# Kernel tuning notes

Measured on AMD Instinct MI355X. Metric: run time of the kernel, lower is better.

## Reference

```python
import jax, jax.numpy as jnp
import numpy as np

SCORE = 89; PERF = 300; R = SCORE + PERF   # roll_dims = score_1hot + perf_1hot
H = 1024; Z = 256; B = 64; T = 256
DUR, DY, IOI = 0, 100, 200                 # perf segment boundaries (durratio/dy/ioi)
BN_EPS = 1e-5

PARAM_SHAPES = [
    ("w_ih_f", (3*H, R)), ("w_hh_f", (3*H, H)), ("b_ih_f", (3*H,)), ("b_hh_f", (3*H,)),
    ("w_ih_b", (3*H, R)), ("w_hh_b", (3*H, H)), ("b_ih_b", (3*H,)), ("b_hh_b", (3*H,)),
    ("w_mu", (Z, 2*H)), ("b_mu", (Z,)), ("w_var", (Z, 2*H)), ("b_var", (Z,)),
    ("w_init", (H, Z)), ("b_init", (H,)),
    ("w_ih0", (3*H, Z + R)), ("w_hh0", (3*H, H)), ("b_ih0", (3*H,)), ("b_hh0", (3*H,)),
    ("w_ih1", (3*H, H)), ("w_hh1", (3*H, H)), ("b_ih1", (3*H,)), ("b_hh1", (3*H,)),
    ("w_ih2", (3*H, H)), ("w_hh2", (3*H, H)), ("b_ih2", (3*H,)), ("b_hh2", (3*H,)),
    ("w_out", (PERF, H)), ("b_out", (PERF,)),
]


def gru_cell(x, h, w_ih, w_hh, b_ih, b_hh):
    # torch GRU/GRUCell gate order: r, z, n
    gi = x @ w_ih.T + b_ih
    gh = h @ w_hh.T + b_hh
    i_r, i_z, i_n = jnp.split(gi, 3, axis=-1)
    h_r, h_z, h_n = jnp.split(gh, 3, axis=-1)
    r = jax.nn.sigmoid(i_r + h_r)
    zg = jax.nn.sigmoid(i_z + h_z)
    n = jnp.tanh(i_n + r * h_n)
    return (1.0 - zg) * n + zg * h


def setup_inputs() -> dict:
    key = jax.random.key(0)
    ks = jax.random.split(key, len(PARAM_SHAPES) + 1)
    inp = {"x": jax.random.normal(ks[0], (T, B, R), dtype=jnp.float32),
           "x_lengths": T}
    for i, (nm, shp) in enumerate(PARAM_SHAPES):
        inp[nm] = jax.random.normal(ks[i + 1], shp, dtype=jnp.float32) * 0.05
    return inp


def _forward(x, w_ih_f, w_hh_f, b_ih_f, b_hh_f, w_ih_b, w_hh_b, b_ih_b, b_hh_b,
             w_mu, b_mu, w_var, b_var, w_init, b_init,
             w_ih0, w_hh0, b_ih0, b_hh0, w_ih1, w_hh1, b_ih1, b_hh1,
             w_ih2, w_hh2, b_ih2, b_hh2, w_out, b_out):
    # ---- encode: bidirectional GRU, all lengths == T (pack == plain GRU) ----
    h0 = jnp.zeros((B, H), x.dtype)
    def run(xs, w_ih, w_hh, b_ih, b_hh):
        step = lambda h, xt: ((gru_cell(xt, h, w_ih, w_hh, b_ih, b_hh),) * 2)
        hT, _ = jax.lax.scan(step, h0, xs)
        return hT
    h_f = run(x, w_ih_f, w_hh_f, b_ih_f, b_hh_f)
    h_b = run(x[::-1], w_ih_b, w_hh_b, b_ih_b, b_hh_b)
    hidden = jnp.concatenate([h_f, h_b], axis=-1)          # [B, 2H]
    hidden = hidden / jnp.sqrt(1.0 + BN_EPS)               # BatchNorm2d(1) eval, fresh running stats
    mean = hidden @ w_mu.T + b_mu
    stddev = jnp.exp((hidden @ w_var.T + b_var) * 0.5)     # computed as in torch (unused in eval)
    z = mean                                               # eval-mode reparameterize -> mean
    score = x[:, :, :SCORE]                                # [T, B, SCORE]
    out0 = jnp.zeros((B, PERF), x.dtype).at[:, -1].set(1.0)
    sc0 = jnp.zeros((B, SCORE), x.dtype).at[:, -1].set(1.0)
    hinit = jnp.tanh(z @ w_init.T + b_init)                # hx[0] init
    def step(carry, xj):
        out, sc, hx0, hx1, hx2 = carry
        j, score_j = xj
        inp = jnp.concatenate([out, sc, z], axis=1)        # [B, PERF+SCORE+Z]
        hx0 = gru_cell(inp, hx0, w_ih0, w_hh0, b_ih0, b_hh0)
        hx1 = gru_cell(hx0, jnp.where(j == 0, hx0, hx1), w_ih1, w_hh1, b_ih1, b_hh1)
        hx2 = gru_cell(hx1, jnp.where(j == 0, hx1, hx2), w_ih2, w_hh2, b_ih2, b_hh2)
        logits = hx2 @ w_out.T + b_out                     # [B, PERF]
        o = jnp.concatenate([jax.nn.log_softmax(logits[:, DUR:DY], axis=1),
                             jax.nn.log_softmax(logits[:, DY:IOI], axis=1),
                             jax.nn.log_softmax(logits[:, IOI:], axis=1)], axis=1)
        out_next = jax.nn.one_hot(jnp.argmax(o, axis=1), PERF, dtype=o.dtype)  # eval sampling
        return (out_next, score_j, hx0, hx1, hx2), o
    _, outs = jax.lax.scan(step, (out0, sc0, hinit, hinit, hinit),
                           (jnp.arange(T), score))
    return outs.transpose(1, 0, 2)                         # [B, T, PERF]


def reference(x, x_lengths, w_ih_f, w_hh_f, b_ih_f, b_hh_f, w_ih_b, w_hh_b, b_ih_b, b_hh_b,
              w_mu, b_mu, w_var, b_var, w_init, b_init,
              w_ih0, w_hh0, b_ih0, b_hh0, w_ih1, w_hh1, b_ih1, b_hh1,
              w_ih2, w_hh2, b_ih2, b_hh2, w_out, b_out):
    outs = _forward(x, w_ih_f, w_hh_f, b_ih_f, b_hh_f, w_ih_b, w_hh_b, b_ih_b, b_hh_b,
                    w_mu, b_mu, w_var, b_var, w_init, b_init,
                    w_ih0, w_hh0, b_ih0, b_hh0, w_ih1, w_hh1, b_ih1, b_hh1,
                    w_ih2, w_hh2, b_ih2, b_hh2, w_out, b_out)
    zeros = jnp.zeros((B, Z), x.dtype)  # dis_mean / dis_stddev stay zero in eval branch
    return outs, zeros, zeros
```

## Files before the change

kernel.cpp:

```cpp
#include <hip/hip_runtime.h>
#include <math.h>

namespace {

typedef unsigned long long u64;

constexpr int cH  = 1024;
constexpr int cZ  = 256;
constexpr int cB  = 64;
constexpr int cT  = 256;
constexpr int cR  = 389;
constexpr int cSC = 89;
constexpr int cPF = 300;
constexpr int WSTR = 400;
constexpr float INV_S = 0.9999950000374997f;

__device__ __forceinline__ void fma4(float4& a, const float4 x, const float4 w){
  a.x = fmaf(x.x, w.x, a.x);
  a.y = fmaf(x.y, w.y, a.y);
  a.z = fmaf(x.z, w.z, a.z);
  a.w = fmaf(x.w, w.w, a.w);
}
__device__ __forceinline__ float fold4(const float4 a){ return (a.x + a.y) + (a.z + a.w); }
__device__ __forceinline__ float4 z4(){ return make_float4(0.f, 0.f, 0.f, 0.f); }
__device__ __forceinline__ float sigm(float x){ return 1.f / (1.f + expf(-x)); }

__device__ __forceinline__ void cfence(){ asm volatile("" ::: "memory"); }
__device__ __forceinline__ u64 ld_u64(const u64* p){
  return __hip_atomic_load(p, __ATOMIC_RELAXED, __HIP_MEMORY_SCOPE_AGENT);
}
__device__ __forceinline__ float ld_scal(const float* p){
  return __hip_atomic_load(p, __ATOMIC_RELAXED, __HIP_MEMORY_SCOPE_AGENT);
}
__device__ __forceinline__ void st_scal(float* p, float v){
  __hip_atomic_store(p, v, __ATOMIC_RELAXED, __HIP_MEMORY_SCOPE_AGENT);
}

__device__ __forceinline__ void gbarN(unsigned* base, int sub, unsigned subCnt,
                                      int nsub, unsigned rootCnt){
  __syncthreads();
  if (threadIdx.x == 0){
    cfence();
    unsigned* root = base + nsub * 16;
    unsigned* gen  = base + nsub * 16 + 16;
    const unsigned g = __hip_atomic_load(gen, __ATOMIC_RELAXED, __HIP_MEMORY_SCOPE_AGENT);
    const unsigned a = __hip_atomic_fetch_add(base + sub * 16, 1u,
                         __ATOMIC_RELEASE, __HIP_MEMORY_SCOPE_AGENT);
    bool flip = false;
    if (a == subCnt - 1u){
      const unsigned r = __hip_atomic_fetch_add(root, 1u,
                           __ATOMIC_RELEASE, __HIP_MEMORY_SCOPE_AGENT);
      if (r == rootCnt - 1u){
        for (int t = 0; t < nsub; ++t)
          __hip_atomic_store(base + t * 16, 0u, __ATOMIC_RELAXED, __HIP_MEMORY_SCOPE_AGENT);
        __hip_atomic_store(root, 0u, __ATOMIC_RELAXED, __HIP_MEMORY_SCOPE_AGENT);
        __hip_atomic_store(gen, g + 1u, __ATOMIC_RELEASE, __HIP_MEMORY_SCOPE_AGENT);
        flip = true;
      }
    }
    if (!flip){
      while (__hip_atomic_load(gen, __ATOMIC_RELAXED, __HIP_MEMORY_SCOPE_AGENT) == g)
        __builtin_amdgcn_s_sleep(1);
    }
    cfence();
  }
  __syncthreads();
}

__global__ __launch_bounds__(256) void init_kernel(float* hf0, float* hb0, float* dout_tail,
                                                   unsigned* barE, unsigned* barD){
  const int idx = blockIdx.x * 256 + threadIdx.x;
  const int stride = gridDim.x * 256;
  for (int i = idx; i < cB * cH; i += stride){ hf0[i] = 0.f; hb0[i] = 0.f; }
  for (int i = idx; i < 2 * cB * cZ; i += stride) dout_tail[i] = 0.f;
  for (int i = idx; i < 2048; i += stride) barE[i] = 0u;
  for (int i = idx; i < 512;  i += stride) barD[i] = 0u;
}

__global__ __launch_bounds__(256) void pad_wih_kernel(const float* __restrict__ w,
                                                      float* __restrict__ wp){
  const int idx = blockIdx.x * 256 + threadIdx.x;
  const int stride = gridDim.x * 256;
  const int n = 3 * cH * WSTR;
  for (int i = idx; i < n; i += stride){
    const int r = i / WSTR, c = i - r * WSTR;
    wp[i] = (c < cR) ? w[(size_t)r * cR + c] : 0.f;
  }
}

__global__ __launch_bounds__(256) void pad_wsc_kernel(const float* __restrict__ w_ih0,
                                                      float* __restrict__ wsc){
  const int idx = blockIdx.x * 256 + threadIdx.x;
  const int stride = gridDim.x * 256;
  const int n = 3 * cH * 96;
  for (int i = idx; i < n; i += stride){
    const int r = i / 96, c = i - r * 96;
    wsc[i] = (c < cSC) ? w_ih0[(size_t)r * 645 + 300 + c] : 0.f;
  }
}

__global__ __launch_bounds__(512, 2) void enc_persist(
    const float* __restrict__ x,
    const float* __restrict__ wihPf, const float* __restrict__ whh_f,
    const float* __restrict__ bih_f, const float* __restrict__ bhh_f,
    const float* __restrict__ wihPb, const float* __restrict__ whh_b,
    const float* __restrict__ bih_b, const float* __restrict__ bhh_b,
    float* __restrict__ hfA, float* __restrict__ hfB,
    float* __restrict__ hbA, float* __restrict__ hbB,
    unsigned* __restrict__ barE)
{
  const int bid   = blockIdx.x;
  const int xcd   = bid & 7;
  const int slot  = bid >> 3;
  const int dir   = slot >> 4;
  const int sub16 = slot & 15;
  const int kblk  = xcd * 8 + (sub16 >> 1);
  const int bhalf = sub16 & 1;
  unsigned* bar   = barE + (dir * 2 + bhalf) * 512;

  const float* wih = dir ? wihPb : wihPf;
  const float* whh = dir ? whh_b : whh_f;
  const float* bih = dir ? bih_b : bih_f;
  const float* bhh = dir ? bhh_b : bhh_f;
  float* bufA = dir ? hbA : hfA;
  float* bufB = dir ? hbB : hfB;

  const int tid   = threadIdx.x;
  const int seg8  = tid >> 6;
  const int dseg  = seg8 & 3;
  const int khalf = seg8 >> 2;
  const int lane  = tid & 63;
  const int tx    = lane & 7;
  const int ty    = lane >> 3;
  const int k0    = kblk * 16;
  const int bbase = bhalf * 32;
  const int kloc  = khalf * 8 + ty;
  const int k     = k0 + kloc;

  __shared__ float part[4][4][16][33];
  __shared__ alignas(16) float sh[32 * 516];

  const float4* w0i = (const float4*)wih + (size_t)k * 100;
  const float4* w1i = (const float4*)wih + (size_t)(cH + k) * 100;
  const float4* w2i = (const float4*)wih + (size_t)(2*cH + k) * 100;
  const float4* w0h = (const float4*)whh + (size_t)k * 256;
  const float4* w1h = (const float4*)whh + (size_t)(cH + k) * 256;
  const float4* w2h = (const float4*)whh + (size_t)(2*cH + k) * 256;
  float4* sh4 = (float4*)sh;

  auto stageE = [&](const float* hin, int p){
    const u64* s8 = (const u64*)hin;
    u64* d8 = (u64*)sh;
    u64 tmp[16];
    #pragma unroll
    for (int i = 0; i < 16; ++i){
      const int e = i * 512 + tid;
      tmp[i] = ld_u64(s8 + (size_t)(bbase + (e >> 8)) * 512 + p * 256 + (e & 255));
    }
    #pragma unroll
    for (int i = 0; i < 16; ++i){
      const int e = i * 512 + tid;
      d8[(e >> 8) * 258 + (e & 255)] = tmp[i];
    }
  };

  for (int t = 0; t < cT; ++t){
    const float* hin = (t & 1) ? bufB : bufA;
    float*      hout = (t & 1) ? bufA : bufB;
    const int tt = dir ? (cT - 1 - t) : t;

    float4 R[4], Z[4], NI[4], NH[4];
    #pragma unroll
    for (int jj = 0; jj < 4; ++jj){ R[jj]=z4(); Z[jj]=z4(); NI[jj]=z4(); NH[jj]=z4(); }

    {
      const float* xb[4];
      #pragma unroll
      for (int jj = 0; jj < 4; ++jj)
        xb[jj] = x + ((size_t)tt * cB + bbase + tx + 8*jj) * cR;
      const int c0 = dseg * 25;
      const int cEnd = c0 + 25;
      const int cSafe = (cEnd < 97) ? cEnd : 97;
      for (int c = c0; c < cSafe; ++c){
        const float4 w0v = w0i[c], w1v = w1i[c], w2v = w2i[c];
        const int d = 4 * c;
        #pragma unroll
        for (int jj = 0; jj < 4; ++jj){
          const float* xr = xb[jj];
          const float4 a = make_float4(xr[d], xr[d+1], xr[d+2], xr[d+3]);
          fma4(R[jj], a, w0v); fma4(Z[jj], a, w1v); fma4(NI[jj], a, w2v);
        }
      }
      for (int c = cSafe; c < cEnd; ++c){
        const float4 w0v = w0i[c], w1v = w1i[c], w2v = w2i[c];
        const int d = 4 * c;
        #pragma unroll
        for (int jj = 0; jj < 4; ++jj){
          const float* xr = xb[jj];
          const float4 a = make_float4(
              (d   < cR) ? xr[d]   : 0.f, (d+1 < cR) ? xr[d+1] : 0.f,
              (d+2 < cR) ? xr[d+2] : 0.f, (d+3 < cR) ? xr[d+3] : 0.f);
          fma4(R[jj], a, w0v); fma4(Z[jj], a, w1v); fma4(NI[jj], a, w2v);
        }
      }
    }

    #pragma unroll 1
    for (int p = 0; p < 2; ++p){
      stageE(hin, p);
      __syncthreads();
      {
        const float4* wp0 = w0h + p * 128;
        const float4* wp1 = w1h + p * 128;
        const float4* wp2 = w2h + p * 128;
        #pragma unroll 4
        for (int c = 0; c < 32; ++c){
          const int cc = dseg * 32 + c;
          const float4 w0v = wp0[cc], w1v = wp1[cc], w2v = wp2[cc];
          #pragma unroll
          for (int jj = 0; jj < 4; ++jj){
            const float4 a = sh4[(tx + 8*jj)*129 + cc];
            fma4(R[jj], a, w0v); fma4(Z[jj], a, w1v); fma4(NH[jj], a, w2v);
          }
        }
      }
      __syncthreads();
    }

    #pragma unroll
    for (int jj = 0; jj < 4; ++jj){
      const int b = tx + 8*jj;
      part[dseg][0][kloc][b] = fold4(R[jj]);
      part[dseg][1][kloc][b] = fold4(Z[jj]);
      part[dseg][2][kloc][b] = fold4(NI[jj]);
      part[dseg][3][kloc][b] = fold4(NH[jj]);
    }
    __syncthreads();
    {
      const int row = tid >> 5, bb = tid & 31;
      float rs=0.f, zs=0.f, nis=0.f, nhs=0.f;
      #pragma unroll
      for (int s = 0; s < 4; ++s){
        rs += part[s][0][row][bb]; zs += part[s][1][row][bb];
        nis += part[s][2][row][bb]; nhs += part[s][3][row][bb];
      }
      const int kk = k0 + row, gb = bbase + bb;
      const float r  = sigm(rs + bih[kk] + bhh[kk]);
      const float zg = sigm(zs + bih[cH + kk] + bhh[cH + kk]);
      const float nn = tanhf(nis + bih[2*cH + kk] + r * (nhs + bhh[2*cH + kk]));
      const float hp = ld_scal(&hin[(size_t)gb * cH + kk]);
      st_scal(&hout[(size_t)gb * cH + kk], (1.f - zg) * nn + zg * hp);
    }
    gbarN(bar, kblk >> 3, 8u, 8, 8u);
  }
}

__global__ __launch_bounds__(512, 2) void dec_persist(
    const float* __restrict__ x,
    const float* __restrict__ hfA, const float* __restrict__ hbA,
    const float* __restrict__ w_mu, const float* __restrict__ b_mu,
    const float* __restrict__ w_init, const float* __restrict__ b_init,
    const float* __restrict__ w_ih0,
    const float* __restrict__ wsc,   const float* __restrict__ w_hh0,
    const float* __restrict__ b_ih0, const float* __restrict__ b_hh0,
    const float* __restrict__ w_ih1, const float* __restrict__ w_hh1,
    const float* __restrict__ b_ih1, const float* __restrict__ b_hh1,
    const float* __restrict__ w_ih2, const float* __restrict__ w_hh2,
    const float* __restrict__ b_ih2, const float* __restrict__ b_hh2,
    const float* __restrict__ w_out, const float* __restrict__ b_out,
    float* __restrict__ h0A, float* __restrict__ h0B,
    float* __restrict__ h1A, float* __restrict__ h1B,
    float* __restrict__ h2A, float* __restrict__ h2B,
    float* __restrict__ gi0z, float* __restrict__ zbuf,
    float* __restrict__ amg,  float* __restrict__ scg,
    float* __restrict__ dout,
    unsigned* __restrict__ barD)
{
  const int bid  = blockIdx.x;
  const int xcd  = bid & 7;
  const int slot = bid >> 3;
  const int kq   = xcd * 16 + (slot >> 1);
  const int bh   = slot & 1;
  const int kbase = kq * 8;
  const int bbase = bh * 32;
  const int tid = threadIdx.x;

  const int seg  = tid >> 6;
  const int lane = tid & 63;
  const int tx   = lane & 7;
  const int ty   = lane >> 3;
  const int k    = kbase + ty;

  __shared__ float part[8][4][8][33];
  __shared__ alignas(16) float stg[16 * 1028];
  __shared__ alignas(16) float scs[32 * 100];
  __shared__ float ams[32];
  __shared__ alignas(16) float hb2[cH];
  __shared__ float lg[cPF];
  __shared__ float gmax[3], glse[3], wbest[8];
  __shared__ int   wbidx[8];

  float4* stg4 = (float4*)stg;

  #define GBD gbarN(barD, bid >> 4, 16u, 16, 16u)

  auto stageH = [&](const float* src, int gb0){
    const u64* s8 = (const u64*)src;
    u64* d8 = (u64*)stg;
    u64 tmp[16];
    #pragma unroll
    for (int i = 0; i < 16; ++i){
      const int e = i * 512 + tid;
      tmp[i] = ld_u64(s8 + (size_t)(gb0 + (e >> 9)) * 512 + (e & 511));
    }
    #pragma unroll
    for (int i = 0; i < 16; ++i){
      const int e = i * 512 + tid;
      d8[(e >> 9) * 514 + (e & 511)] = tmp[i];
    }
  };

  auto accH = [&](const float4* w0, const float4* w1, const float4* w2,
                  float4& A0, float4& A1, float4& B0, float4& B1,
                  float4& C0, float4& C1){
    #pragma unroll 4
    for (int c = 0; c < 32; ++c){
      const int cc = seg * 32 + c;
      const float4 w0v = w0[cc], w1v = w1[cc], w2v = w2[cc];
      const float4 aA = stg4[tx * 257 + cc];
      const float4 aB = stg4[(tx + 8) * 257 + cc];
      fma4(A0, aA, w0v); fma4(B0, aA, w1v); fma4(C0, aA, w2v);
      fma4(A1, aB, w0v); fma4(B1, aB, w1v); fma4(C1, aB, w2v);
    }
  };

  auto reduce_store = [&](const float* bi, const float* bhv,
                          const float* hprev, float* hout){
    __syncthreads();
    if (tid < 256){
      const int row = tid >> 5, b = tid & 31;
      float rs=0.f, zs=0.f, nis=0.f, nhs=0.f;
      #pragma unroll
      for (int s = 0; s < 8; ++s){
        rs += part[s][0][row][b]; zs += part[s][1][row][b];
        nis += part[s][2][row][b]; nhs += part[s][3][row][b];
      }
      const int kk = kbase + row, gb = bbase + b;
      const float r  = sigm(rs + bi[kk] + bhv[kk]);
      const float zg = sigm(zs + bi[cH + kk] + bhv[cH + kk]);
      const float nn = tanhf(nis + bi[2*cH + kk] + r * (nhs + bhv[2*cH + kk]));
      const float hp = ld_scal(&hprev[(size_t)gb * cH + kk]);
      st_scal(&hout[(size_t)gb * cH + kk], (1.f - zg) * nn + zg * hp);
    }
  };

  if (bid < cB){
    const int b = bid;
    float4* hl4 = (float4*)stg;
    hl4[tid] = (tid < 256) ? ((const float4*)hfA)[(size_t)b * 256 + tid]
                           : ((const float4*)hbA)[(size_t)b * 256 + (tid - 256)];
    __syncthreads();
    if (tid < 256){
      const float4* wr = (const float4*)w_mu + (size_t)tid * 512;
      float4 s = z4();
      #pragma unroll 4
      for (int c = 0; c < 512; ++c) fma4(s, hl4[c], wr[c]);
      st_scal(&zbuf[(size_t)b * cZ + tid], b_mu[tid] + fold4(s) * INV_S);
    }
    if (tid == 0) st_scal(&amg[b], 299.f);
    if (tid < 96) st_scal(&scg[(size_t)b * 96 + tid], (tid == 88) ? 1.f : 0.f);
  }
  GBD;
  {
    float* zl = stg;
    {
      u64 tmp[8];
      const u64* zb8 = (const u64*)zbuf;
      u64* zl8 = (u64*)stg;
      #pragma unroll
      for (int q = 0; q < 8; ++q){
        const int e = q * 512 + tid;
        tmp[q] = ld_u64(zb8 + (size_t)(bbase + (e >> 7)) * 128 + (e & 127));
      }
      #pragma unroll
      for (int q = 0; q < 8; ++q){
        const int e = q * 512 + tid;
        zl8[(e >> 7) * 130 + (e & 127)] = tmp[q];
      }
    }
    __syncthreads();
    for (int e = tid; e < 768; e += 512){
      const int g = e >> 8, kr = (e >> 5) & 7, b = e & 31;
      const float* zr = zl + b * 260;
      const float* wrow = w_ih0 + (size_t)(g * cH + kbase + kr) * 645 + 389;
      float s = 0.f;
      #pragma unroll 4
      for (int d = 0; d < cZ; ++d) s = fmaf(zr[d], wrow[d], s);
      st_scal(&gi0z[(size_t)(g * cH + kbase + kr) * 64 + bbase + b], s);
    }
    if (tid < 256){
      const int kr = tid >> 5, b = tid & 31;
      const float4* zr4 = (const float4*)(zl + b * 260);
      const float4* wr4 = (const float4*)w_init + (size_t)(kbase + kr) * 64;
      float4 s = z4();
      #pragma unroll 4
      for (int d = 0; d < 64; ++d) fma4(s, zr4[d], wr4[d]);
      st_scal(&h0A[(size_t)(bbase + b) * cH + kbase + kr],
              tanhf(b_init[kbase + kr] + fold4(s)));
    }
  }
  GBD;

  for (int j = 0; j < cT; ++j){
    const int par = j & 1;
    const float* h0p = par ? h0B : h0A;  float* h0n = par ? h0A : h0B;
    const float* h1p = par ? h1B : h1A;  float* h1n = par ? h1A : h1B;
    const float* h2p = par ? h2B : h2A;  float* h2n = par ? h2A : h2B;

    {
      {
        u64 tmp[3];
        const u64* sg8 = (const u64*)scg;
        u64* sc8 = (u64*)scs;
        #pragma unroll
        for (int i = 0; i < 3; ++i){
          const int e = i * 512 + tid;
          const int row = e / 48, col = e - row * 48;
          tmp[i] = ld_u64(sg8 + (size_t)(bbase + row) * 48 + col);
        }
        #pragma unroll
        for (int i = 0; i < 3; ++i){
          const int e = i * 512 + tid;
          const int row = e / 48, col = e - row * 48;
          sc8[row * 50 + col] = tmp[i];
        }
        if (tid < 32) ams[tid] = ld_scal(&amg[bbase + tid]);
      }
      __syncthreads();

      float4 R[4], Z[4], NI[4], NH[4];
      float sR[4], sZ[4], sNI[4];
      #pragma unroll
      for (int jj = 0; jj < 4; ++jj){
        R[jj]=z4(); Z[jj]=z4(); NI[jj]=z4(); NH[jj]=z4();
        sR[jj]=0.f; sZ[jj]=0.f; sNI[jj]=0.f;
      }
      {
        const float4* ws0 = (const float4*)wsc + (size_t)k * 24;
        const float4* ws1 = (const float4*)wsc + (size_t)(cH + k) * 24;
        const float4* ws2 = (const float4*)wsc + (size_t)(2*cH + k) * 24;
        const float4* sc4 = (const float4*)scs;
        #pragma unroll
        for (int c = 0; c < 3; ++c){
          const int cc = seg * 3 + c;
          const float4 w0v = ws0[cc], w1v = ws1[cc], w2v = ws2[cc];
          #pragma unroll
          for (int jj = 0; jj < 4; ++jj){
            const float4 a = sc4[(tx + 8*jj) * 25 + cc];
            fma4(R[jj], a, w0v); fma4(Z[jj], a, w1v); fma4(NI[jj], a, w2v);
          }
        }
      }
      if (seg == 0){
        #pragma unroll
        for (int jj = 0; jj < 4; ++jj){
          const int b = tx + 8*jj, gb = bbase + b;
          const int am = (int)ams[b];
          sR[jj]  = w_ih0[(size_t)k * 645 + am]
                  + ld_scal(&gi0z[(size_t)k * 64 + gb]);
          sZ[jj]  = w_ih0[(size_t)(cH + k) * 645 + am]
                  + ld_scal(&gi0z[(size_t)(cH + k) * 64 + gb]);
          sNI[jj] = w_ih0[(size_t)(2*cH + k) * 645 + am]
                  + ld_scal(&gi0z[(size_t)(2*cH + k) * 64 + gb]);
        }
      }
      const float4* wh0 = (const float4*)w_hh0 + (size_t)k * 256;
      const float4* wh1 = (const float4*)w_hh0 + (size_t)(cH + k) * 256;
      const float4* wh2 = (const float4*)w_hh0 + (size_t)(2*cH + k) * 256;
      __syncthreads();
      stageH(h0p, bbase);      __syncthreads();
      accH(wh0, wh1, wh2, R[0], R[1], Z[0], Z[1], NH[0], NH[1]);
      __syncthreads();
      stageH(h0p, bbase + 16); __syncthreads();
      accH(wh0, wh1, wh2, R[2], R[3], Z[2], Z[3], NH[2], NH[3]);
      #pragma unroll
      for (int jj = 0; jj < 4; ++jj){
        const int b = tx + 8*jj;
        part[seg][0][ty][b] = fold4(R[jj]) + sR[jj];
        part[seg][1][ty][b] = fold4(Z[jj]) + sZ[jj];
        part[seg][2][ty][b] = fold4(NI[jj]) + sNI[jj];
        part[seg][3][ty][b] = fold4(NH[jj]);
      }
      reduce_store(b_ih0, b_hh0, h0p, h0n);
    }
    GBD;

    #pragma unroll 1
    for (int L = 0; L < 2; ++L){
      const float* inG = (L == 0) ? h0n : h1n;
      const float* pvG = (L == 0) ? (j == 0 ? h0n : h1p) : (j == 0 ? h1n : h2p);
      const float* wih = (L == 0) ? w_ih1 : w_ih2;
      const float* whh = (L == 0) ? w_hh1 : w_hh2;
      const float* bi  = (L == 0) ? b_ih1 : b_ih2;
      const float* bhv = (L == 0) ? b_hh1 : b_hh2;
      float* outG      = (L == 0) ? h1n : h2n;

      float4 R[4], Z[4], NI[4], NH[4];
      #pragma unroll
      for (int jj = 0; jj < 4; ++jj){ R[jj]=z4(); Z[jj]=z4(); NI[jj]=z4(); NH[jj]=z4(); }
      const float4* wi0 = (const float4*)wih + (size_t)k * 256;
      const float4* wi1 = (const float4*)wih + (size_t)(cH + k) * 256;
      const float4* wi2 = (const float4*)wih + (size_t)(2*cH + k) * 256;
      const float4* wh0 = (const float4*)whh + (size_t)k * 256;
      const float4* wh1 = (const float4*)whh + (size_t)(cH + k) * 256;
      const float4* wh2 = (const float4*)whh + (size_t)(2*cH + k) * 256;

      stageH(inG, bbase);      __syncthreads();
      accH(wi0, wi1, wi2, R[0], R[1], Z[0], Z[1], NI[0], NI[1]);
      __syncthreads();
      stageH(inG, bbase + 16); __syncthreads();
      accH(wi0, wi1, wi2, R[2], R[3], Z[2], Z[3], NI[2], NI[3]);
      __syncthreads();
      stageH(pvG, bbase);      __syncthreads();
      accH(wh0, wh1, wh2, R[0], R[1], Z[0], Z[1], NH[0], NH[1]);
      __syncthreads();
      stageH(pvG, bbase + 16); __syncthreads();
      accH(wh0, wh1, wh2, R[2], R[3], Z[2], Z[3], NH[2], NH[3]);
      #pragma unroll
      for (int jj = 0; jj < 4; ++jj){
        const int b = tx + 8*jj;
        part[seg][0][ty][b] = fold4(R[jj]);
        part[seg][1][ty][b] = fold4(Z[jj]);
        part[seg][2][ty][b] = fold4(NI[jj]);
        part[seg][3][ty][b] = fold4(NH[jj]);
      }
      reduce_store(bi, bhv, pvG, outG);
      GBD;
    }

    if (bid < cB){
      const int b = bid;
      ((u64*)hb2)[tid] = ld_u64((const u64*)h2n + (size_t)b * 512 + tid);
      __syncthreads();
      for (int p = tid; p < cPF; p += 512){
        const float4* wr = (const float4*)w_out + (size_t)p * 256;
        const float4* hv = (const float4*)hb2;
        float4 s = z4();
        #pragma unroll 4
        for (int c = 0; c < 256; ++c) fma4(s, hv[c], wr[c]);
        lg[p] = b_out[p] + fold4(s);
      }
      __syncthreads();
      const int w = tid >> 6, l = tid & 63;
      if (w < 3){
        float m = -INFINITY;
        for (int p = w*100 + l; p < w*100 + 100; p += 64) m = fmaxf(m, lg[p]);
        #pragma unroll
        for (int off = 32; off > 0; off >>= 1) m = fmaxf(m, __shfl_xor(m, off));
        float s = 0.f;
        for (int p = w*100 + l; p < w*100 + 100; p += 64) s += expf(lg[p] - m);
        #pragma unroll
        for (int off = 32; off > 0; off >>= 1) s += __shfl_xor(s, off);
        if (l == 0){ gmax[w] = m; glse[w] = logf(s); }
      }
      __syncthreads();
      float best = -INFINITY; int bidx = 0x7fffffff;
      for (int p = tid; p < cPF; p += 512){
        const int g3 = (p >= 200) ? 2 : ((p >= 100) ? 1 : 0);
        const float o = lg[p] - gmax[g3] - glse[g3];
        dout[((size_t)b * cT + j) * cPF + p] = o;
        if (o > best || (o == best && p < bidx)){ best = o; bidx = p; }
      }
      #pragma unroll
      for (int off = 32; off > 0; off >>= 1){
        const float ob = __shfl_xor(best, off);
        const int   oi = __shfl_xor(bidx, off);
        if (ob > best || (ob == best && oi < bidx)){ best = ob; bidx = oi; }
      }
      if (l == 0){ wbest[w] = best; wbidx[w] = bidx; }
      __syncthreads();
      if (tid == 0){
        float bb = wbest[0]; int bi = wbidx[0];
        #pragma unroll
        for (int q = 1; q < 8; ++q)
          if (wbest[q] > bb || (wbest[q] == bb && wbidx[q] < bi)){ bb = wbest[q]; bi = wbidx[q]; }
        st_scal(&amg[b], (float)bi);
      }
      if (tid < 96)
        st_scal(&scg[(size_t)b * 96 + tid],
                (tid < cSC) ? x[((size_t)j * cB + b) * cR + tid] : 0.f);
    }
    GBD;
  }
  #undef GBD
}

}

extern "C" void kernel_launch(void* const* d_in, const int* in_sizes, int n_in,
                              void* d_out, int out_size, void* d_ws, size_t ws_size,
                              hipStream_t stream)
{
  const float* x     = (const float*)d_in[0];
  const float* wih_f = (const float*)d_in[2];
  const float* whh_f = (const float*)d_in[3];
  const float* bih_f = (const float*)d_in[4];
  const float* bhh_f = (const float*)d_in[5];
  const float* wih_b = (const float*)d_in[6];
  const float* whh_b = (const float*)d_in[7];
  const float* bih_b = (const float*)d_in[8];
  const float* bhh_b = (const float*)d_in[9];
  const float* w_mu  = (const float*)d_in[10];
  const float* b_mu  = (const float*)d_in[11];
  const float* w_init= (const float*)d_in[14];
  const float* b_init= (const float*)d_in[15];
  const float* w_ih0 = (const float*)d_in[16];
  const float* w_hh0 = (const float*)d_in[17];
  const float* b_ih0 = (const float*)d_in[18];
  const float* b_hh0 = (const float*)d_in[19];
  const float* w_ih1 = (const float*)d_in[20];
  const float* w_hh1 = (const float*)d_in[21];
  const float* b_ih1 = (const float*)d_in[22];
  const float* b_hh1 = (const float*)d_in[23];
  const float* w_ih2 = (const float*)d_in[24];
  const float* w_hh2 = (const float*)d_in[25];
  const float* b_ih2 = (const float*)d_in[26];
  const float* b_hh2 = (const float*)d_in[27];
  const float* w_out = (const float*)d_in[28];
  const float* b_out = (const float*)d_in[29];
  float* dout = (float*)d_out;

  float* ws = (float*)d_ws;
  float* wihfP = ws; ws += (size_t)3 * cH * WSTR;
  float* wihbP = ws; ws += (size_t)3 * cH * WSTR;
  float* wsc   = ws; ws += (size_t)3 * cH * 96;
  float* gi0z  = ws; ws += (size_t)3 * cH * 64;
  float* hfA = ws; ws += cB * cH;  float* hfB = ws; ws += cB * cH;
  float* hbA = ws; ws += cB * cH;  float* hbB = ws; ws += cB * cH;
  float* h0A = ws; ws += cB * cH;  float* h0B = ws; ws += cB * cH;
  float* h1A = ws; ws += cB * cH;  float* h1B = ws; ws += cB * cH;
  float* h2A = ws; ws += cB * cH;  float* h2B = ws; ws += cB * cH;
  float* zbuf = ws; ws += cB * cZ;
  float* scg  = ws; ws += cB * 96;
  float* amg  = ws; ws += cB;
  ws = (float*)(((uintptr_t)ws + 255) & ~(uintptr_t)255);
  unsigned* barE = (unsigned*)ws;  ws += 2048;
  unsigned* barD = (unsigned*)ws;  ws += 512;

  init_kernel<<<256, 256, 0, stream>>>(hfA, hbA, dout + (size_t)cB * cT * cPF, barE, barD);
  pad_wih_kernel<<<512, 256, 0, stream>>>(wih_f, wihfP);
  pad_wih_kernel<<<512, 256, 0, stream>>>(wih_b, wihbP);
  pad_wsc_kernel<<<512, 256, 0, stream>>>(w_ih0, wsc);

  enc_persist<<<256, 512, 0, stream>>>(
      x,
      wihfP, whh_f, bih_f, bhh_f,
      wihbP, whh_b, bih_b, bhh_b,
      hfA, hfB, hbA, hbB, barE);

  dec_persist<<<256, 512, 0, stream>>>(
      x, hfA, hbA,
      w_mu, b_mu, w_init, b_init,
      w_ih0, wsc, w_hh0, b_ih0, b_hh0,
      w_ih1, w_hh1, b_ih1, b_hh1,
      w_ih2, w_hh2, b_ih2, b_hh2,
      w_out, b_out,
      h0A, h0B, h1A, h1B, h2A, h2B,
      gi0z, zbuf, amg, scg, dout, barD);
}
```

Baseline: 51.21 ms.

## Prefetch next hidden-state tile into registers and split decoder barrier by batch half

Both persistent GRU kernels now split staging into an issue phase (global loads into registers) and a commit phase (register-to-LDS store). This lets the load of the next 16/32-row hidden chunk overlap the FMA loop on the current one. The decoder also replaces its grid-wide barrier with per-batch-half barriers over 128 blocks (barL), and moves the output head to blocks indexed by kq within each half, so the two halves run independently. The barrier region grows to hold the extra counters. This raises register pressure from the 16 u64 staging registers and depends on bh/kq indexing correctly separating the two batch halves.

```diff
diff --git a/kernel.cpp b/kernel.cpp
--- a/kernel.cpp
+++ b/kernel.cpp
@@ -73,8 +73,7 @@
   const int stride = gridDim.x * 256;
   for (int i = idx; i < cB * cH; i += stride){ hf0[i] = 0.f; hb0[i] = 0.f; }
   for (int i = idx; i < 2 * cB * cZ; i += stride) dout_tail[i] = 0.f;
-  for (int i = idx; i < 2048; i += stride) barE[i] = 0u;
-  for (int i = idx; i < 512;  i += stride) barD[i] = 0u;
+  for (int i = idx; i < 2048; i += stride){ barE[i] = 0u; barD[i] = 0u; }
 }
 
 __global__ __launch_bounds__(256) void pad_wih_kernel(const float* __restrict__ w,
@@ -148,19 +147,22 @@
   const float4* w2h = (const float4*)whh + (size_t)(2*cH + k) * 256;
   float4* sh4 = (float4*)sh;
 
-  auto stageE = [&](const float* hin, int p){
+  u64 S[16];
+  auto stage_issue = [&](const float* hin, int p){
     const u64* s8 = (const u64*)hin;
-    u64* d8 = (u64*)sh;
-    u64 tmp[16];
     #pragma unroll
     for (int i = 0; i < 16; ++i){
       const int e = i * 512 + tid;
-      tmp[i] = ld_u64(s8 + (size_t)(bbase + (e >> 8)) * 512 + p * 256 + (e & 255));
-    }
+      S[i] = ld_u64(s8 + (size_t)(bbase + (e >> 8)) * 512 + p * 256 + (e & 255));
+    }
+    cfence();
+  };
+  auto stage_commit = [&](){
+    u64* d8 = (u64*)sh;
     #pragma unroll
     for (int i = 0; i < 16; ++i){
       const int e = i * 512 + tid;
-      d8[(e >> 8) * 258 + (e & 255)] = tmp[i];
+      d8[(e >> 8) * 258 + (e & 255)] = S[i];
     }
   };
 
@@ -172,6 +174,8 @@
     float4 R[4], Z[4], NI[4], NH[4];
     #pragma unroll
     for (int jj = 0; jj < 4; ++jj){ R[jj]=z4(); Z[jj]=z4(); NI[jj]=z4(); NH[jj]=z4(); }
+
+    stage_issue(hin, 0);
 
     {
       const float* xb[4];
@@ -205,27 +209,43 @@
       }
     }
 
-    #pragma unroll 1
-    for (int p = 0; p < 2; ++p){
-      stageE(hin, p);
-      __syncthreads();
-      {
-        const float4* wp0 = w0h + p * 128;
-        const float4* wp1 = w1h + p * 128;
-        const float4* wp2 = w2h + p * 128;
-        #pragma unroll 4
-        for (int c = 0; c < 32; ++c){
-          const int cc = dseg * 32 + c;
-          const float4 w0v = wp0[cc], w1v = wp1[cc], w2v = wp2[cc];
-          #pragma unroll
-          for (int jj = 0; jj < 4; ++jj){
-            const float4 a = sh4[(tx + 8*jj)*129 + cc];
-            fma4(R[jj], a, w0v); fma4(Z[jj], a, w1v); fma4(NH[jj], a, w2v);
-          }
+    stage_commit();
+    __syncthreads();
+    stage_issue(hin, 1);
+    {
+      const float4* wp0 = w0h;
+      const float4* wp1 = w1h;
+      const float4* wp2 = w2h;
+      #pragma unroll 4
+      for (int c = 0; c < 32; ++c){
+        const int cc = dseg * 32 + c;
+        const float4 w0v = wp0[cc], w1v = wp1[cc], w2v = wp2[cc];
+        #pragma unroll
+        for (int jj = 0; jj < 4; ++jj){
+          const float4 a = sh4[(tx + 8*jj)*129 + cc];
+          fma4(R[jj], a, w0v); fma4(Z[jj], a, w1v); fma4(NH[jj], a, w2v);
         }
       }
-      __syncthreads();
-    }
+    }
+    __syncthreads();
+    stage_commit();
+    __syncthreads();
+    {
+      const float4* wp0 = w0h + 128;
+      const float4* wp1 = w1h + 128;
+      const float4* wp2 = w2h + 128;
+      #pragma unroll 4
+      for (int c = 0; c < 32; ++c){
+        const int cc = dseg * 32 + c;
+        const float4 w0v = wp0[cc], w1v = wp1[cc], w2v = wp2[cc];
+        #pragma unroll
+        for (int jj = 0; jj < 4; ++jj){
+          const float4 a = sh4[(tx + 8*jj)*129 + cc];
+          fma4(R[jj], a, w0v); fma4(Z[jj], a, w1v); fma4(NH[jj], a, w2v);
+        }
+      }
+    }
+    __syncthreads();
 
     #pragma unroll
     for (int jj = 0; jj < 4; ++jj){
@@ -302,21 +322,26 @@
 
   float4* stg4 = (float4*)stg;
 
-  #define GBD gbarN(barD, bid >> 4, 16u, 16, 16u)
-
-  auto stageH = [&](const float* src, int gb0){
+  #define GBD  gbarN(barD, bid >> 4, 16u, 16, 16u)
+  unsigned* barL = barD + 512 + bh * 512;
+  #define GBL  gbarN(barL, kq >> 4, 16u, 8, 8u)
+
+  u64 S[16];
+  auto stage_issue = [&](const float* src, int gb0){
     const u64* s8 = (const u64*)src;
-    u64* d8 = (u64*)stg;
-    u64 tmp[16];
     #pragma unroll
     for (int i = 0; i < 16; ++i){
       const int e = i * 512 + tid;
-      tmp[i] = ld_u64(s8 + (size_t)(gb0 + (e >> 9)) * 512 + (e & 511));
-    }
+      S[i] = ld_u64(s8 + (size_t)(gb0 + (e >> 9)) * 512 + (e & 511));
+    }
+    cfence();
+  };
+  auto stage_commit = [&](){
+    u64* d8 = (u64*)stg;
     #pragma unroll
     for (int i = 0; i < 16; ++i){
       const int e = i * 512 + tid;
-      d8[(e >> 9) * 514 + (e & 511)] = tmp[i];
+      d8[(e >> 9) * 514 + (e & 511)] = S[i];
     }
   };
 
@@ -438,6 +463,8 @@
       }
       __syncthreads();
 
+      stage_issue(h0p, bbase);
+
       float4 R[4], Z[4], NI[4], NH[4];
       float sR[4], sZ[4], sNI[4];
       #pragma unroll
@@ -478,10 +505,11 @@
       const float4* wh1 = (const float4*)w_hh0 + (size_t)(cH + k) * 256;
       const float4* wh2 = (const float4*)w_hh0 + (size_t)(2*cH + k) * 256;
       __syncthreads();
-      stageH(h0p, bbase);      __syncthreads();
+      stage_commit(); __syncthreads();
+      stage_issue(h0p, bbase + 16);
       accH(wh0, wh1, wh2, R[0], R[1], Z[0], Z[1], NH[0], NH[1]);
       __syncthreads();
-      stageH(h0p, bbase + 16); __syncthreads();
+      stage_commit(); __syncthreads();
       accH(wh0, wh1, wh2, R[2], R[3], Z[2], Z[3], NH[2], NH[3]);
       #pragma unroll
       for (int jj = 0; jj < 4; ++jj){
@@ -493,7 +521,7 @@
       }
       reduce_store(b_ih0, b_hh0, h0p, h0n);
     }
-    GBD;
+    GBL;
 
     #pragma unroll 1
     for (int L = 0; L < 2; ++L){
@@ -515,16 +543,20 @@
       const float4* wh1 = (const float4*)whh + (size_t)(cH + k) * 256;
       const float4* wh2 = (const float4*)whh + (size_t)(2*cH + k) * 256;
 
-      stageH(inG, bbase);      __syncthreads();
+      stage_issue(inG, bbase);
+      stage_commit(); __syncthreads();
+      stage_issue(inG, bbase + 16);
       accH(wi0, wi1, wi2, R[0], R[1], Z[0], Z[1], NI[0], NI[1]);
       __syncthreads();
-      stageH(inG, bbase + 16); __syncthreads();
+      stage_commit(); __syncthreads();
+      stage_issue(pvG, bbase);
       accH(wi0, wi1, wi2, R[2], R[3], Z[2], Z[3], NI[2], NI[3]);
       __syncthreads();
-      stageH(pvG, bbase);      __syncthreads();
+      stage_commit(); __syncthreads();
+      stage_issue(pvG, bbase + 16);
       accH(wh0, wh1, wh2, R[0], R[1], Z[0], Z[1], NH[0], NH[1]);
       __syncthreads();
-      stageH(pvG, bbase + 16); __syncthreads();
+      stage_commit(); __syncthreads();
       accH(wh0, wh1, wh2, R[2], R[3], Z[2], Z[3], NH[2], NH[3]);
       #pragma unroll
       for (int jj = 0; jj < 4; ++jj){
@@ -535,11 +567,11 @@
         part[seg][3][ty][b] = fold4(NH[jj]);
       }
       reduce_store(bi, bhv, pvG, outG);
-      GBD;
-    }
-
-    if (bid < cB){
-      const int b = bid;
+      GBL;
+    }
+
+    if (kq < 32){
+      const int b = bbase + kq;
       ((u64*)hb2)[tid] = ld_u64((const u64*)h2n + (size_t)b * 512 + tid);
       __syncthreads();
       for (int p = tid; p < cPF; p += 512){
@@ -590,9 +622,10 @@
         st_scal(&scg[(size_t)b * 96 + tid],
                 (tid < cSC) ? x[((size_t)j * cB + b) * cR + tid] : 0.f);
     }
-    GBD;
+    GBL;
   }
   #undef GBD
+  #undef GBL
 }
 
 }
@@ -645,7 +678,7 @@
   float* amg  = ws; ws += cB;
   ws = (float*)(((uintptr_t)ws + 255) & ~(uintptr_t)255);
   unsigned* barE = (unsigned*)ws;  ws += 2048;
-  unsigned* barD = (unsigned*)ws;  ws += 512;
+  unsigned* barD = (unsigned*)ws;  ws += 2048;
 
   init_kernel<<<256, 256, 0, stream>>>(hfA, hbA, dout + (size_t)cB * cT * cPF, barE, barD);
   pad_wih_kernel<<<512, 256, 0, stream>>>(wih_f, wihfP);
```

Result: slower. 56.44 ms (+10.2%).
